# Performance work log

Hardware: AMD Instinct MI355X
Metric: run time of the kernel (lower is better)

The kernel has to match this reference:

```python
import jax, jax.numpy as jnp
import numpy as np

NUM_LEVELS = 16
LOG2_T = 19
TABLE_SIZE = 1 << LOG2_T
F_PER_LEVEL = 2
MIN_RES, MAX_RES = 16, 4096
N = 524288

_growth = np.exp((np.log(MAX_RES) - np.log(MIN_RES)) / (NUM_LEVELS - 1))
SCALINGS = np.floor(MIN_RES * _growth ** np.arange(NUM_LEVELS)).astype(np.float32)  # [L]
HASH_OFFSET = (np.arange(NUM_LEVELS) * TABLE_SIZE).astype(np.uint32)  # [L]
# corner selection: True -> use ceil coord, order matches torch hashed_0..hashed_7
CORNER_MASK = np.array([[1,1,1],[1,0,1],[0,0,1],[0,1,1],[1,1,0],[1,0,0],[0,0,0],[0,1,0]], dtype=bool)
PRIMES = np.array([1, 2654435761, 805459861], dtype=np.uint32)


def _hash(coords):
    # coords: uint32 [..., 3]; instant-ngp spatial hash, table size is a power of 2
    c = coords * jnp.asarray(PRIMES)
    h = c[..., 0] ^ c[..., 1] ^ c[..., 2]
    h = h & jnp.uint32(TABLE_SIZE - 1)
    return (h + jnp.asarray(HASH_OFFSET)).astype(jnp.int32)  # [..., L]


def hash_encode(pts, table):
    # pts: [N, 3] in [0,1]; table: [L*T, F]
    scaled = pts[:, None, :] * jnp.asarray(SCALINGS)[:, None]            # [N, L, 3]
    sc = jnp.ceil(scaled).astype(jnp.int32).astype(jnp.uint32)
    sf_f = jnp.floor(scaled)
    sf = sf_f.astype(jnp.int32).astype(jnp.uint32)
    offset = scaled - sf_f                                               # [N, L, 3]
    mask = jnp.asarray(CORNER_MASK)[:, None, None, :]                    # [8,1,1,3]
    coords = jnp.where(mask, sc[None], sf[None])                         # [8, N, L, 3]
    f = table[_hash(coords)]                                             # [8, N, L, F]
    wx = offset[..., 0:1]; wy = offset[..., 1:2]; wz = offset[..., 2:3]
    f_03 = f[0] * wx + f[3] * (1 - wx)
    f_12 = f[1] * wx + f[2] * (1 - wx)
    f_56 = f[5] * wx + f[6] * (1 - wx)
    f_47 = f[4] * wx + f[7] * (1 - wx)
    f0312 = f_03 * wy + f_12 * (1 - wy)
    f4756 = f_47 * wy + f_56 * (1 - wy)
    enc = f0312 * wz + f4756 * (1 - wz)                                  # [N, L, F]
    return enc.reshape(enc.shape[0], NUM_LEVELS * F_PER_LEVEL)


def setup_inputs() -> dict:
    key = jax.random.key(0)
    k1, k2, k3, k4 = jax.random.split(key, 4)
    x = jax.random.uniform(k1, (N, 6), dtype=jnp.float32)
    hash_table = (jax.random.uniform(k2, (TABLE_SIZE * NUM_LEVELS, F_PER_LEVEL), dtype=jnp.float32) * 2 - 1) * 1e-3
    w1 = jax.random.normal(k3, (64, 64), dtype=jnp.float32) * 0.05
    w2 = jax.random.normal(k4, (64, 16), dtype=jnp.float32) * 0.05
    return {"x": x, "hash_table": hash_table, "w1": w1, "w2": w2}


def reference(x, hash_table, w1, w2):
    p0, p1 = x[:, :3], x[:, 3:]                          # segment start / end
    enc = jnp.concatenate([hash_encode(p0, hash_table), hash_encode(p1, hash_table)], axis=-1)  # [N,64]
    h = jax.nn.relu(enc @ w1)                            # FullyFusedMLP: 1 hidden layer, ReLU, no bias
    out = h @ w2                                         # [N, 1+geo_feat_dim]
    density = jnp.exp(out[:, :1] - 1.0)                  # trunc_exp(x - 1)
    return jnp.concatenate([density, out[:, 1:]], axis=-1)
```

## Files before the change

### kernel.cpp

```cpp
#include <hip/hip_runtime.h>
#include <math.h>

#define NLVL 16
#define TSIZE (1u << 19)
#define PRIME_Y 2654435761u
#define PRIME_Z 805459861u
#define QSCALE 126000.0f
#define W1SCALE 254.0f

#if __has_builtin(__builtin_amdgcn_sdot4)
#define HAS_SDOT4 1
#else
#define HAS_SDOT4 0
#endif
#if __has_builtin(__builtin_amdgcn_fdot2)
#define HAS_FDOT2 1
#else
#define HAS_FDOT2 0
#endif

typedef _Float16 half2_t __attribute__((ext_vector_type(2)));

struct ScalingsArg { float s[NLVL]; };
struct QuadArg { int off[4]; int res[4]; };

__device__ __forceinline__ unsigned f2bf(float f) {
    unsigned u = __float_as_uint(f);
    return (u + 0x7fffu + ((u >> 16) & 1u)) >> 16;
}
__device__ __forceinline__ float bf2f(unsigned hw) { return __uint_as_float(hw << 16); }
__device__ __forceinline__ unsigned pkbf2(float2 v) { return f2bf(v.x) | (f2bf(v.y) << 16); }

__device__ __forceinline__ int q8(float v) {
    return __float2int_rn(fmaxf(fminf(v * QSCALE, 127.f), -127.f));
}
__device__ __forceinline__ unsigned qw8(float v) {
    return (unsigned)(__float2int_rn(fmaxf(fminf(v * W1SCALE, 127.f), -127.f))) & 0xffu;
}

__device__ __forceinline__ int dot4i8(unsigned a, unsigned b, int c) {
#if HAS_SDOT4
    return __builtin_amdgcn_sdot4((int)a, (int)b, c, false);
#else
    c += (int)(signed char)(a & 0xffu)         * (int)(signed char)(b & 0xffu);
    c += (int)(signed char)((a >> 8) & 0xffu)  * (int)(signed char)((b >> 8) & 0xffu);
    c += (int)(signed char)((a >> 16) & 0xffu) * (int)(signed char)((b >> 16) & 0xffu);
    c += (int)(signed char)(a >> 24)           * (int)(signed char)(b >> 24);
    return c;
#endif
}

__device__ __forceinline__ unsigned pkh2(float a, float b) {
    union { half2_t h; unsigned u; } cv;
    cv.h.x = (_Float16)a; cv.h.y = (_Float16)b;
    return cv.u;
}
__device__ __forceinline__ float dot2h(unsigned a, unsigned b, float c) {
    union { unsigned u; half2_t h; } ca, cb;
    ca.u = a; cb.u = b;
#if HAS_FDOT2
    return __builtin_amdgcn_fdot2(ca.h, cb.h, c, false);
#else
    return c + (float)ca.h.x * (float)cb.h.x + (float)ca.h.y * (float)cb.h.y;
#endif
}

__device__ __forceinline__ unsigned pick4(uint4 q, int sel) {
    const unsigned a = (sel & 1) ? q.y : q.x;
    const unsigned b = (sel & 1) ? q.w : q.z;
    return (sel & 2) ? b : a;
}

__global__ __launch_bounds__(256) void ngp_conv12(
    const float4* __restrict__ src, uint2* __restrict__ o, int n2)
{
    const int i = blockIdx.x * 256 + threadIdx.x;
    if (i < n2) {
        const float4 v = src[i];
        o[i] = make_uint2(f2bf(v.x) | (f2bf(v.y) << 16),
                          f2bf(v.z) | (f2bf(v.w) << 16));
    }
}

__global__ __launch_bounds__(256) void ngp_quad(
    const float2* __restrict__ tf, uint4* __restrict__ quads, QuadArg qa)
{
    const int l = blockIdx.y;
    const int res = qa.res[l];
    const int n = (res + 1) * res * res;
    const int idx = blockIdx.x * 256 + threadIdx.x;
    if (idx >= n) return;
    const int xq = idx % res;
    const int t1 = idx / res;
    const int yq = t1 % res;
    const int zq = t1 / res;
    const unsigned m = TSIZE - 1u;
    const unsigned base = (unsigned)l * TSIZE;
    const unsigned hy0 = (unsigned)yq * PRIME_Y, hy1 = (unsigned)(yq + 1) * PRIME_Y;
    const unsigned hz  = (unsigned)zq * PRIME_Z;
    const unsigned x0 = (unsigned)xq, x1 = (unsigned)(xq + 1);
    const float2 e00 = tf[((x0 ^ hy0 ^ hz) & m) + base];
    const float2 e10 = tf[((x1 ^ hy0 ^ hz) & m) + base];
    const float2 e01 = tf[((x0 ^ hy1 ^ hz) & m) + base];
    const float2 e11 = tf[((x1 ^ hy1 ^ hz) & m) + base];
    quads[qa.off[l] + idx] = make_uint4(pkbf2(e00), pkbf2(e10), pkbf2(e01), pkbf2(e11));
}

__global__ __launch_bounds__(256) void ngp_encode2(
    const float* __restrict__ x,
    const unsigned* __restrict__ tbHi,
    const uint4* __restrict__ quads,
    unsigned* __restrict__ encq,
    ScalingsArg sca, QuadArg qa, int npts)
{
    const int pt = blockIdx.x * 256 + threadIdx.x;
    if (pt >= npts) return;
    const int l = blockIdx.y;
    const float s = sca.s[l];
    const unsigned m = TSIZE - 1u;

    const float* xp = x + (size_t)pt * 6;
    const float2 v0 = *reinterpret_cast<const float2*>(xp);
    const float2 v1 = *reinterpret_cast<const float2*>(xp + 2);
    const float2 v2 = *reinterpret_cast<const float2*>(xp + 4);
    const float q[2][3] = { { v0.x, v0.y, v1.x }, { v1.y, v2.x, v2.y } };

    int qb[4];
    #pragma unroll
    for (int e = 0; e < 2; ++e) {
        const float sx = q[e][0] * s, sy = q[e][1] * s, sz = q[e][2] * s;
        const float fx = floorf(sx), fy = floorf(sy), fz = floorf(sz);
        const float wx = sx - fx, wy = sy - fy, wz = sz - fz;
        const unsigned ixf = (unsigned)(int)fx, iyf = (unsigned)(int)fy, izf = (unsigned)(int)fz;
        const unsigned ixc = (unsigned)(int)ceilf(sx);
        const unsigned iyc = (unsigned)(int)ceilf(sy);
        const unsigned izc = (unsigned)(int)ceilf(sz);

        float2 cc[4], cf[4];

        if (l < 4) {
            const int res = qa.res[l];
            const int dxs = (int)(ixc - ixf);
            const int dys = (int)(iyc - iyf);
            const uint4* Q = quads + qa.off[l];
            const int rowf = (int)iyf * res + (int)ixf;
            const uint4 qzc = Q[(int)izc * (res * res) + rowf];
            const uint4 qzf = Q[(int)izf * (res * res) + rowf];
            const int selcc = dys * 2 + dxs;
            const int selfc = dys * 2;
            const int selcf = dxs;
            const unsigned u0 = pick4(qzc, selcc);
            const unsigned u1 = pick4(qzc, selcf);
            const unsigned u2 = qzc.x;
            const unsigned u3 = pick4(qzc, selfc);
            const unsigned u4 = pick4(qzf, selcc);
            const unsigned u5 = pick4(qzf, selcf);
            const unsigned u6 = qzf.x;
            const unsigned u7 = pick4(qzf, selfc);
            cc[0] = make_float2(bf2f(u0 & 0xffffu), bf2f(u0 >> 16));
            cf[0] = make_float2(bf2f(u3 & 0xffffu), bf2f(u3 >> 16));
            cc[1] = make_float2(bf2f(u1 & 0xffffu), bf2f(u1 >> 16));
            cf[1] = make_float2(bf2f(u2 & 0xffffu), bf2f(u2 >> 16));
            cc[2] = make_float2(bf2f(u5 & 0xffffu), bf2f(u5 >> 16));
            cf[2] = make_float2(bf2f(u6 & 0xffffu), bf2f(u6 >> 16));
            cc[3] = make_float2(bf2f(u4 & 0xffffu), bf2f(u4 >> 16));
            cf[3] = make_float2(bf2f(u7 & 0xffffu), bf2f(u7 >> 16));
        } else {
            const unsigned base = (unsigned)(l - 4) * TSIZE;
            const unsigned hyf = iyf * PRIME_Y, hyc = iyc * PRIME_Y;
            const unsigned hzf = izf * PRIME_Z, hzc = izc * PRIME_Z;
            const unsigned H[4] = { hyc ^ hzc, hyf ^ hzc, hyf ^ hzf, hyc ^ hzf };
            const unsigned dx = ixf ^ ixc;
            #pragma unroll
            for (int j = 0; j < 4; ++j) {
                const unsigned A  = (ixf ^ H[j]) & m;
                const unsigned Ax = A ^ dx;
                const uint4 blk = *reinterpret_cast<const uint4*>(&tbHi[base + (A & ~3u)]);
                const unsigned uf = pick4(blk, (int)(A & 3u));
                unsigned uc = pick4(blk, (int)(Ax & 3u));
                if (dx > 3u) uc = tbHi[base + Ax];
                cf[j] = make_float2(bf2f(uf & 0xffffu), bf2f(uf >> 16));
                cc[j] = make_float2(bf2f(uc & 0xffffu), bf2f(uc >> 16));
            }
        }

        const float cx = 1.f - wx, cy = 1.f - wy, cz = 1.f - wz;
        const float g03x = cc[0].x * wx + cf[0].x * cx, g03y = cc[0].y * wx + cf[0].y * cx;
        const float g12x = cc[1].x * wx + cf[1].x * cx, g12y = cc[1].y * wx + cf[1].y * cx;
        const float g56x = cc[2].x * wx + cf[2].x * cx, g56y = cc[2].y * wx + cf[2].y * cx;
        const float g47x = cc[3].x * wx + cf[3].x * cx, g47y = cc[3].y * wx + cf[3].y * cx;
        const float t0x = g03x * wy + g12x * cy, t0y = g03y * wy + g12y * cy;
        const float t1x = g47x * wy + g56x * cy, t1y = g47y * wy + g56y * cy;
        qb[e * 2 + 0] = q8(t0x * wz + t1x * cz);
        qb[e * 2 + 1] = q8(t0y * wz + t1y * cz);
    }

    encq[(size_t)l * npts + pt] =
        (qb[0] & 0xff) | ((qb[1] & 0xff) << 8) | ((qb[2] & 0xff) << 16) | ((qb[3] & 0xff) << 24);
}

template<int BF>
__global__ __launch_bounds__(256) void ngp_encode_lvl(
    const float* __restrict__ x,
    const float2* __restrict__ tf,
    const unsigned* __restrict__ tb,
    unsigned* __restrict__ encq,
    ScalingsArg sca, int npts)
{
    const int pt = blockIdx.x * 256 + threadIdx.x;
    if (pt >= npts) return;
    const int l = blockIdx.y;
    const float s = sca.s[l];
    const unsigned base = (unsigned)l * TSIZE;
    const unsigned m = TSIZE - 1u;

    const float* xp = x + (size_t)pt * 6;
    const float2 v0 = *reinterpret_cast<const float2*>(xp);
    const float2 v1 = *reinterpret_cast<const float2*>(xp + 2);
    const float2 v2 = *reinterpret_cast<const float2*>(xp + 4);
    const float q[2][3] = { { v0.x, v0.y, v1.x }, { v1.y, v2.x, v2.y } };

    int qb[4];
    #pragma unroll
    for (int e = 0; e < 2; ++e) {
        const float sx = q[e][0] * s, sy = q[e][1] * s, sz = q[e][2] * s;
        const float fx = floorf(sx), fy = floorf(sy), fz = floorf(sz);
        const float wx = sx - fx, wy = sy - fy, wz = sz - fz;
        const unsigned ixf = (unsigned)(int)fx, iyf = (unsigned)(int)fy, izf = (unsigned)(int)fz;
        const unsigned ixc = (unsigned)(int)ceilf(sx);
        const unsigned iyc = (unsigned)(int)ceilf(sy);
        const unsigned izc = (unsigned)(int)ceilf(sz);
        const unsigned hyf = iyf * PRIME_Y, hyc = iyc * PRIME_Y;
        const unsigned hzf = izf * PRIME_Z, hzc = izc * PRIME_Z;
        const unsigned h0 = hyc ^ hzc, h1 = hyf ^ hzc, h2 = hyf ^ hzf, h3 = hyc ^ hzf;
        const unsigned dx = ixf ^ ixc;
        const unsigned A[4] = { (ixf ^ h0) & m, (ixf ^ h1) & m,
                                (ixf ^ h2) & m, (ixf ^ h3) & m };
        float2 cf[4], cc[4];
        if (dx == 1u) {
            #pragma unroll
            for (int j = 0; j < 4; ++j) {
                const float4 v = *reinterpret_cast<const float4*>(&tf[base + (A[j] & ~1u)]);
                const bool hi = (A[j] & 1u) != 0u;
                cf[j] = hi ? make_float2(v.z, v.w) : make_float2(v.x, v.y);
                cc[j] = hi ? make_float2(v.x, v.y) : make_float2(v.z, v.w);
            }
        } else {
            #pragma unroll
            for (int j = 0; j < 4; ++j) {
                cf[j] = tf[base + A[j]];
                cc[j] = tf[base + ((A[j] ^ dx) & m)];
            }
        }
        const float cx = 1.f - wx, cy = 1.f - wy, cz = 1.f - wz;
        const float g03x = cc[0].x * wx + cf[0].x * cx, g03y = cc[0].y * wx + cf[0].y * cx;
        const float g12x = cc[1].x * wx + cf[1].x * cx, g12y = cc[1].y * wx + cf[1].y * cx;
        const float g56x = cc[2].x * wx + cf[2].x * cx, g56y = cc[2].y * wx + cf[2].y * cx;
        const float g47x = cc[3].x * wx + cf[3].x * cx, g47y = cc[3].y * wx + cf[3].y * cx;
        const float t0x = g03x * wy + g12x * cy, t0y = g03y * wy + g12y * cy;
        const float t1x = g47x * wy + g56x * cy, t1y = g47y * wy + g56y * cy;
        qb[e * 2 + 0] = q8(t0x * wz + t1x * cz);
        qb[e * 2 + 1] = q8(t0y * wz + t1y * cz);
    }
    encq[(size_t)l * npts + pt] =
        (qb[0] & 0xff) | ((qb[1] & 0xff) << 8) | ((qb[2] & 0xff) << 16) | ((qb[3] & 0xff) << 24);
}

__global__ __launch_bounds__(256) void ngp_mlp2i(
    const unsigned* __restrict__ encq,
    const float* __restrict__ w1,
    const float* __restrict__ w2,
    float* __restrict__ out, int npts)
{
    __shared__ unsigned lw1i[64 * 16];
    __shared__ unsigned lw2h[16 * 32];
    const int tid = threadIdx.x;

    #pragma unroll
    for (int t = 0; t < 4; ++t) {
        const int idx = tid * 4 + t;
        const int j = idx >> 4, g = idx & 15;
        const unsigned b0 = qw8(w1[(2 * g) * 64 + j]);
        const unsigned b1 = qw8(w1[(2 * g + 1) * 64 + j]);
        const unsigned b2 = qw8(w1[(32 + 2 * g) * 64 + j]);
        const unsigned b3 = qw8(w1[(33 + 2 * g) * 64 + j]);
        lw1i[j * 16 + g] = b0 | (b1 << 8) | (b2 << 16) | (b3 << 24);
    }
    #pragma unroll
    for (int t = 0; t < 2; ++t) {
        const int idx = tid * 2 + t;
        const int c = idx >> 5, jp = idx & 31;
        lw2h[c * 32 + jp] = pkh2(w2[(2 * jp) * 16 + c], w2[(2 * jp + 1) * 16 + c]);
    }
    __syncthreads();

    const int base = (blockIdx.x * 256 + tid) * 2;
    if (base >= npts) return;

    unsigned ev0[16], ev1[16];
    #pragma unroll
    for (int l = 0; l < NLVL; ++l) {
        const uint2 v = *reinterpret_cast<const uint2*>(&encq[(size_t)l * npts + base]);
        ev0[l] = v.x; ev1[l] = v.y;
    }

    const float s1 = 1.0f / (QSCALE * W1SCALE);
    unsigned hp0[32], hp1[32];
    #pragma unroll
    for (int jp = 0; jp < 32; ++jp) {
        const int j0 = 2 * jp, j1 = 2 * jp + 1;
        int a00 = 0, a10 = 0, a01 = 0, a11 = 0;
        #pragma unroll
        for (int g4 = 0; g4 < 4; ++g4) {
            const uint4 w = *reinterpret_cast<const uint4*>(&lw1i[j0 * 16 + g4 * 4]);
            a00 = dot4i8(ev0[g4 * 4 + 0], w.x, a00); a10 = dot4i8(ev1[g4 * 4 + 0], w.x, a10);
            a00 = dot4i8(ev0[g4 * 4 + 1], w.y, a00); a10 = dot4i8(ev1[g4 * 4 + 1], w.y, a10);
            a00 = dot4i8(ev0[g4 * 4 + 2], w.z, a00); a10 = dot4i8(ev1[g4 * 4 + 2], w.z, a10);
            a00 = dot4i8(ev0[g4 * 4 + 3], w.w, a00); a10 = dot4i8(ev1[g4 * 4 + 3], w.w, a10);
        }
        #pragma unroll
        for (int g4 = 0; g4 < 4; ++g4) {
            const uint4 w = *reinterpret_cast<const uint4*>(&lw1i[j1 * 16 + g4 * 4]);
            a01 = dot4i8(ev0[g4 * 4 + 0], w.x, a01); a11 = dot4i8(ev1[g4 * 4 + 0], w.x, a11);
            a01 = dot4i8(ev0[g4 * 4 + 1], w.y, a01); a11 = dot4i8(ev1[g4 * 4 + 1], w.y, a11);
            a01 = dot4i8(ev0[g4 * 4 + 2], w.z, a01); a11 = dot4i8(ev1[g4 * 4 + 2], w.z, a11);
            a01 = dot4i8(ev0[g4 * 4 + 3], w.w, a01); a11 = dot4i8(ev1[g4 * 4 + 3], w.w, a11);
        }
        hp0[jp] = pkh2(fmaxf((float)a00, 0.f) * s1, fmaxf((float)a01, 0.f) * s1);
        hp1[jp] = pkh2(fmaxf((float)a10, 0.f) * s1, fmaxf((float)a11, 0.f) * s1);
    }

    float* op0 = out + (size_t)base * 16;
    const bool p1 = (base + 1 < npts);
    for (int c = 0; c < 16; ++c) {
        float s0 = 0.f, s1v = 0.f;
        #pragma unroll
        for (int jq = 0; jq < 8; ++jq) {
            const uint4 w = *reinterpret_cast<const uint4*>(&lw2h[c * 32 + jq * 4]);
            s0  = dot2h(hp0[jq * 4 + 0], w.x, s0);  s1v = dot2h(hp1[jq * 4 + 0], w.x, s1v);
            s0  = dot2h(hp0[jq * 4 + 1], w.y, s0);  s1v = dot2h(hp1[jq * 4 + 1], w.y, s1v);
            s0  = dot2h(hp0[jq * 4 + 2], w.z, s0);  s1v = dot2h(hp1[jq * 4 + 2], w.z, s1v);
            s0  = dot2h(hp0[jq * 4 + 3], w.w, s0);  s1v = dot2h(hp1[jq * 4 + 3], w.w, s1v);
        }
        if (c == 0) { s0 = expf(s0 - 1.0f); s1v = expf(s1v - 1.0f); }
        op0[c] = s0;
        if (p1) op0[16 + c] = s1v;
    }
}

__global__ __launch_bounds__(256) void ngp_fused(
    const float* __restrict__ x,
    const float2* __restrict__ table,
    const float* __restrict__ w1,
    const float* __restrict__ w2,
    float* __restrict__ out,
    ScalingsArg sca, int npts)
{
    __shared__ float lw1[64 * 64];
    __shared__ float lw2[64 * 16];
    const int tid = threadIdx.x;
    #pragma unroll
    for (int i = 0; i < 16; ++i) lw1[tid + 256 * i] = w1[tid + 256 * i];
    #pragma unroll
    for (int i = 0; i < 4; ++i)  lw2[tid + 256 * i] = w2[tid + 256 * i];
    __syncthreads();

    const int gid = blockIdx.x * 256 + tid;
    if (gid >= npts) return;

    const float* xp = x + (size_t)gid * 6;
    float2 v0 = *reinterpret_cast<const float2*>(xp);
    float2 v1 = *reinterpret_cast<const float2*>(xp + 2);
    float2 v2 = *reinterpret_cast<const float2*>(xp + 4);
    float Pt[6] = { v0.x, v0.y, v1.x, v1.y, v2.x, v2.y };

    float enc[64];
    #pragma unroll
    for (int p = 0; p < 2; ++p) {
        const float qx = Pt[p * 3 + 0], qy = Pt[p * 3 + 1], qz = Pt[p * 3 + 2];
        #pragma unroll
        for (int l = 0; l < NLVL; ++l) {
            const float s = sca.s[l];
            const float sx = qx * s, sy = qy * s, sz = qz * s;
            const float fx = floorf(sx), fy = floorf(sy), fz = floorf(sz);
            const float wx = sx - fx, wy = sy - fy, wz = sz - fz;
            const unsigned ixf = (unsigned)(int)fx, iyf = (unsigned)(int)fy, izf = (unsigned)(int)fz;
            const unsigned ixc = (unsigned)(int)ceilf(sx);
            const unsigned iyc = (unsigned)(int)ceilf(sy);
            const unsigned izc = (unsigned)(int)ceilf(sz);
            const unsigned hyf = iyf * PRIME_Y, hyc = iyc * PRIME_Y;
            const unsigned hzf = izf * PRIME_Z, hzc = izc * PRIME_Z;
            const unsigned mm = TSIZE - 1u;
            const unsigned bs = (unsigned)l * TSIZE;
            const float2 f0 = table[((ixc ^ hyc ^ hzc) & mm) + bs];
            const float2 f1 = table[((ixc ^ hyf ^ hzc) & mm) + bs];
            const float2 f2 = table[((ixf ^ hyf ^ hzc) & mm) + bs];
            const float2 f3 = table[((ixf ^ hyc ^ hzc) & mm) + bs];
            const float2 f4 = table[((ixc ^ hyc ^ hzf) & mm) + bs];
            const float2 f5 = table[((ixc ^ hyf ^ hzf) & mm) + bs];
            const float2 f6 = table[((ixf ^ hyf ^ hzf) & mm) + bs];
            const float2 f7 = table[((ixf ^ hyc ^ hzf) & mm) + bs];
            const float cx = 1.f - wx, cy = 1.f - wy, cz = 1.f - wz;
            const float g03x = f0.x * wx + f3.x * cx, g03y = f0.y * wx + f3.y * cx;
            const float g12x = f1.x * wx + f2.x * cx, g12y = f1.y * wx + f2.y * cx;
            const float g56x = f5.x * wx + f6.x * cx, g56y = f5.y * wx + f6.y * cx;
            const float g47x = f4.x * wx + f7.x * cx, g47y = f4.y * wx + f7.y * cx;
            const float t0x = g03x * wy + g12x * cy, t0y = g03y * wy + g12y * cy;
            const float t1x = g47x * wy + g56x * cy, t1y = g47y * wy + g56y * cy;
            enc[p * 32 + l * 2 + 0] = t0x * wz + t1x * cz;
            enc[p * 32 + l * 2 + 1] = t0y * wz + t1y * cz;
        }
    }

    float o[16];
    #pragma unroll
    for (int i = 0; i < 16; ++i) o[i] = 0.f;
    for (int jb = 0; jb < 64; jb += 8) {
        float acc[8];
        #pragma unroll
        for (int jj = 0; jj < 8; ++jj) acc[jj] = 0.f;
        #pragma unroll
        for (int k = 0; k < 64; ++k) {
            const float e = enc[k];
            const float4* wrow = reinterpret_cast<const float4*>(&lw1[k * 64 + jb]);
            const float4 wa = wrow[0], wb = wrow[1];
            acc[0] += e * wa.x; acc[1] += e * wa.y; acc[2] += e * wa.z; acc[3] += e * wa.w;
            acc[4] += e * wb.x; acc[5] += e * wb.y; acc[6] += e * wb.z; acc[7] += e * wb.w;
        }
        #pragma unroll
        for (int jj = 0; jj < 8; ++jj) {
            const float hv = fmaxf(acc[jj], 0.f);
            const float4* w2row = reinterpret_cast<const float4*>(&lw2[(jb + jj) * 16]);
            const float4 wa = w2row[0], wb = w2row[1], wc = w2row[2], wd = w2row[3];
            o[0]  += hv * wa.x; o[1]  += hv * wa.y; o[2]  += hv * wa.z; o[3]  += hv * wa.w;
            o[4]  += hv * wb.x; o[5]  += hv * wb.y; o[6]  += hv * wb.z; o[7]  += hv * wb.w;
            o[8]  += hv * wc.x; o[9]  += hv * wc.y; o[10] += hv * wc.z; o[11] += hv * wc.w;
            o[12] += hv * wd.x; o[13] += hv * wd.y; o[14] += hv * wd.z; o[15] += hv * wd.w;
        }
    }
    o[0] = expf(o[0] - 1.0f);
    float4* op = reinterpret_cast<float4*>(out + (size_t)gid * 16);
    op[0] = make_float4(o[0],  o[1],  o[2],  o[3]);
    op[1] = make_float4(o[4],  o[5],  o[6],  o[7]);
    op[2] = make_float4(o[8],  o[9],  o[10], o[11]);
    op[3] = make_float4(o[12], o[13], o[14], o[15]);
}

extern "C" void kernel_launch(void* const* d_in, const int* in_sizes, int n_in,
                              void* d_out, int out_size, void* d_ws, size_t ws_size,
                              hipStream_t stream) {
    const float*  x     = (const float*)d_in[0];
    const float2* table = (const float2*)d_in[1];
    const float*  w1    = (const float*)d_in[2];
    const float*  w2    = (const float*)d_in[3];
    float* out = (float*)d_out;
    const int npts = in_sizes[0] / 6;

    ScalingsArg sca;
    const double growth = exp((log(4096.0) - log(16.0)) / 15.0);
    for (int i = 0; i < NLVL; ++i)
        sca.s[i] = (float)floor(16.0 * pow(growth, (double)i));

    QuadArg qa;
    int qtot = 0, qmax = 0;
    for (int l = 0; l < 4; ++l) {
        const int r = (int)sca.s[l];
        qa.res[l] = r;
        qa.off[l] = qtot;
        const int n = (r + 1) * r * r;
        qtot += n;
        if (n > qmax) qmax = n;
    }

    const size_t tbhi_bytes = (size_t)12 * TSIZE * 4u;
    const size_t enc_bytes  = (size_t)NLVL * (size_t)npts * 4u;
    const size_t quad_bytes = (size_t)qtot * 16u;
    const int bpl = (npts + 255) / 256;
    const dim3 gEnc(bpl, NLVL);
    const int mlp_blocks = ((npts + 1) / 2 + 255) / 256;

    if (ws_size >= tbhi_bytes + enc_bytes + quad_bytes) {
        unsigned* tbHi = (unsigned*)d_ws;
        unsigned* enc  = (unsigned*)((char*)d_ws + tbhi_bytes);
        uint4*    quads = (uint4*)((char*)d_ws + tbhi_bytes + enc_bytes);
        const int n2 = (12 * TSIZE) / 2;
        ngp_conv12<<<(n2 + 255) / 256, 256, 0, stream>>>(
            (const float4*)(table + (size_t)4 * TSIZE), (uint2*)tbHi, n2);
        ngp_quad<<<dim3((qmax + 255) / 256, 4), 256, 0, stream>>>(table, quads, qa);
        ngp_encode2<<<gEnc, 256, 0, stream>>>(x, tbHi, quads, enc, sca, qa, npts);
        ngp_mlp2i<<<mlp_blocks, 256, 0, stream>>>(enc, w1, w2, out, npts);
    } else if (ws_size >= enc_bytes) {
        unsigned* enc = (unsigned*)d_ws;
        ngp_encode_lvl<0><<<gEnc, 256, 0, stream>>>(x, table, nullptr, enc, sca, npts);
        ngp_mlp2i<<<mlp_blocks, 256, 0, stream>>>(enc, w1, w2, out, npts);
    } else {
        ngp_fused<<<(npts + 255) / 256, 256, 0, stream>>>(x, table, w1, w2, out, sca, npts);
    }
}
```

Before: 363.6 us.

## Process two points per thread in encode and extend quad tables to level 4

Replaces the one-point-per-thread encode kernel with one that handles two points per thread. Coordinates are loaded with float4 reads, all gather addresses are computed before the loads, and results are written as a uint2, so more table gathers are in flight per thread. Level 4 also moves from the hashed bf16 table to a precomputed quad table, cutting gathers per corner pair from four to two. The cost is a larger quad workspace, higher register pressure and half as many threads per level.

```diff
diff --git a/kernel.cpp b/kernel.cpp
--- a/kernel.cpp
+++ b/kernel.cpp
@@ -7,6 +7,7 @@
 #define PRIME_Z 805459861u
 #define QSCALE 126000.0f
 #define W1SCALE 254.0f
+#define NQUAD 5
 
 #if __has_builtin(__builtin_amdgcn_sdot4)
 #define HAS_SDOT4 1
@@ -22,7 +23,7 @@
 typedef _Float16 half2_t __attribute__((ext_vector_type(2)));
 
 struct ScalingsArg { float s[NLVL]; };
-struct QuadArg { int off[4]; int res[4]; };
+struct QuadArg { int off[NQUAD]; int res[NQUAD]; };
 
 __device__ __forceinline__ unsigned f2bf(float f) {
     unsigned u = __float_as_uint(f);
@@ -69,6 +70,19 @@
     const unsigned a = (sel & 1) ? q.y : q.x;
     const unsigned b = (sel & 1) ? q.w : q.z;
     return (sel & 2) ? b : a;
+}
+
+__device__ __forceinline__ void lerp8(const float2 cc[4], const float2 cf[4],
+                                      float wx, float wy, float wz, int& qx, int& qy) {
+    const float cx = 1.f - wx, cy = 1.f - wy, cz = 1.f - wz;
+    const float g03x = cc[0].x * wx + cf[0].x * cx, g03y = cc[0].y * wx + cf[0].y * cx;
+    const float g12x = cc[1].x * wx + cf[1].x * cx, g12y = cc[1].y * wx + cf[1].y * cx;
+    const float g56x = cc[2].x * wx + cf[2].x * cx, g56y = cc[2].y * wx + cf[2].y * cx;
+    const float g47x = cc[3].x * wx + cf[3].x * cx, g47y = cc[3].y * wx + cf[3].y * cx;
+    const float t0x = g03x * wy + g12x * cy, t0y = g03y * wy + g12y * cy;
+    const float t1x = g47x * wy + g56x * cy, t1y = g47y * wy + g56y * cy;
+    qx = q8(t0x * wz + t1x * cz);
+    qy = q8(t0y * wz + t1y * cz);
 }
 
 __global__ __launch_bounds__(256) void ngp_conv12(
@@ -106,57 +120,78 @@
     quads[qa.off[l] + idx] = make_uint4(pkbf2(e00), pkbf2(e10), pkbf2(e01), pkbf2(e11));
 }
 
-__global__ __launch_bounds__(256) void ngp_encode2(
+__global__ __launch_bounds__(256) void ngp_encode3(
     const float* __restrict__ x,
     const unsigned* __restrict__ tbHi,
     const uint4* __restrict__ quads,
     unsigned* __restrict__ encq,
     ScalingsArg sca, QuadArg qa, int npts)
 {
-    const int pt = blockIdx.x * 256 + threadIdx.x;
-    if (pt >= npts) return;
+    const int p0 = (blockIdx.x * 256 + threadIdx.x) * 2;
+    if (p0 >= npts) return;
+    const bool has1 = (p0 + 1) < npts;
     const int l = blockIdx.y;
     const float s = sca.s[l];
     const unsigned m = TSIZE - 1u;
 
-    const float* xp = x + (size_t)pt * 6;
-    const float2 v0 = *reinterpret_cast<const float2*>(xp);
-    const float2 v1 = *reinterpret_cast<const float2*>(xp + 2);
-    const float2 v2 = *reinterpret_cast<const float2*>(xp + 4);
-    const float q[2][3] = { { v0.x, v0.y, v1.x }, { v1.y, v2.x, v2.y } };
-
-    int qb[4];
-    #pragma unroll
-    for (int e = 0; e < 2; ++e) {
-        const float sx = q[e][0] * s, sy = q[e][1] * s, sz = q[e][2] * s;
-        const float fx = floorf(sx), fy = floorf(sy), fz = floorf(sz);
-        const float wx = sx - fx, wy = sy - fy, wz = sz - fz;
-        const unsigned ixf = (unsigned)(int)fx, iyf = (unsigned)(int)fy, izf = (unsigned)(int)fz;
-        const unsigned ixc = (unsigned)(int)ceilf(sx);
-        const unsigned iyc = (unsigned)(int)ceilf(sy);
-        const unsigned izc = (unsigned)(int)ceilf(sz);
-
-        float2 cc[4], cf[4];
-
-        if (l < 4) {
-            const int res = qa.res[l];
-            const int dxs = (int)(ixc - ixf);
-            const int dys = (int)(iyc - iyf);
-            const uint4* Q = quads + qa.off[l];
-            const int rowf = (int)iyf * res + (int)ixf;
-            const uint4 qzc = Q[(int)izc * (res * res) + rowf];
-            const uint4 qzf = Q[(int)izf * (res * res) + rowf];
-            const int selcc = dys * 2 + dxs;
-            const int selfc = dys * 2;
-            const int selcf = dxs;
-            const unsigned u0 = pick4(qzc, selcc);
-            const unsigned u1 = pick4(qzc, selcf);
-            const unsigned u2 = qzc.x;
-            const unsigned u3 = pick4(qzc, selfc);
-            const unsigned u4 = pick4(qzf, selcc);
-            const unsigned u5 = pick4(qzf, selcf);
-            const unsigned u6 = qzf.x;
-            const unsigned u7 = pick4(qzf, selfc);
+    const float* xp = x + (size_t)p0 * 6;
+    float SX[4], SY[4], SZ[4];
+    {
+        float c[12];
+        if (has1) {
+            const float4 a0 = *reinterpret_cast<const float4*>(xp);
+            const float4 a1 = *reinterpret_cast<const float4*>(xp + 4);
+            const float4 a2 = *reinterpret_cast<const float4*>(xp + 8);
+            c[0] = a0.x; c[1] = a0.y; c[2]  = a0.z; c[3]  = a0.w;
+            c[4] = a1.x; c[5] = a1.y; c[6]  = a1.z; c[7]  = a1.w;
+            c[8] = a2.x; c[9] = a2.y; c[10] = a2.z; c[11] = a2.w;
+        } else {
+            #pragma unroll
+            for (int i = 0; i < 6; ++i) c[i] = xp[i];
+            #pragma unroll
+            for (int i = 0; i < 6; ++i) c[6 + i] = c[i];
+        }
+        SX[0] = c[0] * s; SY[0] = c[1] * s;  SZ[0] = c[2] * s;
+        SX[1] = c[3] * s; SY[1] = c[4] * s;  SZ[1] = c[5] * s;
+        SX[2] = c[6] * s; SY[2] = c[7] * s;  SZ[2] = c[8] * s;
+        SX[3] = c[9] * s; SY[3] = c[10] * s; SZ[3] = c[11] * s;
+    }
+
+    int qf0[4], qf1[4];
+
+    if (l < NQUAD) {
+        const int res = qa.res[l];
+        const uint4* Q = quads + qa.off[l];
+        uint4 pzc[4], pzf[4];
+        int dxs[4], dys[4];
+        float WX[4], WY[4], WZ[4];
+        #pragma unroll
+        for (int cI = 0; cI < 4; ++cI) {
+            const float sx = SX[cI], sy = SY[cI], sz = SZ[cI];
+            const float fx = floorf(sx), fy = floorf(sy), fz = floorf(sz);
+            WX[cI] = sx - fx; WY[cI] = sy - fy; WZ[cI] = sz - fz;
+            const int ixf = (int)fx, iyf = (int)fy, izf = (int)fz;
+            dxs[cI] = (int)ceilf(sx) - ixf;
+            dys[cI] = (int)ceilf(sy) - iyf;
+            const int izc = (int)ceilf(sz);
+            const int rowf = iyf * res + ixf;
+            pzc[cI] = Q[izc * (res * res) + rowf];
+            pzf[cI] = Q[izf * (res * res) + rowf];
+        }
+        #pragma unroll
+        for (int cI = 0; cI < 4; ++cI) {
+            const int selcc = dys[cI] * 2 + dxs[cI];
+            const int selfc = dys[cI] * 2;
+            const int selcf = dxs[cI];
+            const unsigned u0 = pick4(pzc[cI], selcc);
+            const unsigned u1 = pick4(pzc[cI], selcf);
+            const unsigned u2 = pzc[cI].x;
+            const unsigned u3 = pick4(pzc[cI], selfc);
+            const unsigned u4 = pick4(pzf[cI], selcc);
+            const unsigned u5 = pick4(pzf[cI], selcf);
+            const unsigned u6 = pzf[cI].x;
+            const unsigned u7 = pick4(pzf[cI], selfc);
+            float2 cc[4], cf[4];
             cc[0] = make_float2(bf2f(u0 & 0xffffu), bf2f(u0 >> 16));
             cf[0] = make_float2(bf2f(u3 & 0xffffu), bf2f(u3 >> 16));
             cc[1] = make_float2(bf2f(u1 & 0xffffu), bf2f(u1 >> 16));
@@ -165,38 +200,73 @@
             cf[2] = make_float2(bf2f(u6 & 0xffffu), bf2f(u6 >> 16));
             cc[3] = make_float2(bf2f(u4 & 0xffffu), bf2f(u4 >> 16));
             cf[3] = make_float2(bf2f(u7 & 0xffffu), bf2f(u7 >> 16));
-        } else {
-            const unsigned base = (unsigned)(l - 4) * TSIZE;
-            const unsigned hyf = iyf * PRIME_Y, hyc = iyc * PRIME_Y;
-            const unsigned hzf = izf * PRIME_Z, hzc = izc * PRIME_Z;
-            const unsigned H[4] = { hyc ^ hzc, hyf ^ hzc, hyf ^ hzf, hyc ^ hzf };
-            const unsigned dx = ixf ^ ixc;
-            #pragma unroll
-            for (int j = 0; j < 4; ++j) {
-                const unsigned A  = (ixf ^ H[j]) & m;
-                const unsigned Ax = A ^ dx;
-                const uint4 blk = *reinterpret_cast<const uint4*>(&tbHi[base + (A & ~3u)]);
-                const unsigned uf = pick4(blk, (int)(A & 3u));
-                unsigned uc = pick4(blk, (int)(Ax & 3u));
-                if (dx > 3u) uc = tbHi[base + Ax];
-                cf[j] = make_float2(bf2f(uf & 0xffffu), bf2f(uf >> 16));
-                cc[j] = make_float2(bf2f(uc & 0xffffu), bf2f(uc >> 16));
+            lerp8(cc, cf, WX[cI], WY[cI], WZ[cI], qf0[cI], qf1[cI]);
+        }
+    } else {
+        const unsigned base = (unsigned)(l - 4) * TSIZE;
+        #pragma unroll
+        for (int h = 0; h < 2; ++h) {
+            unsigned A[2][4], DX[2];
+            float WX[2], WY[2], WZ[2];
+            #pragma unroll
+            for (int u = 0; u < 2; ++u) {
+                const int cI = 2 * h + u;
+                const float sx = SX[cI], sy = SY[cI], sz = SZ[cI];
+                const float fx = floorf(sx), fy = floorf(sy), fz = floorf(sz);
+                WX[u] = sx - fx; WY[u] = sy - fy; WZ[u] = sz - fz;
+                const unsigned ixf = (unsigned)(int)fx;
+                const unsigned iyf = (unsigned)(int)fy;
+                const unsigned izf = (unsigned)(int)fz;
+                const unsigned ixc = (unsigned)(int)ceilf(sx);
+                const unsigned iyc = (unsigned)(int)ceilf(sy);
+                const unsigned izc = (unsigned)(int)ceilf(sz);
+                const unsigned hyf = iyf * PRIME_Y, hyc = iyc * PRIME_Y;
+                const unsigned hzf = izf * PRIME_Z, hzc = izc * PRIME_Z;
+                DX[u] = ixf ^ ixc;
+                A[u][0] = (ixf ^ (hyc ^ hzc)) & m;
+                A[u][1] = (ixf ^ (hyf ^ hzc)) & m;
+                A[u][2] = (ixf ^ (hyf ^ hzf)) & m;
+                A[u][3] = (ixf ^ (hyc ^ hzf)) & m;
             }
-        }
-
-        const float cx = 1.f - wx, cy = 1.f - wy, cz = 1.f - wz;
-        const float g03x = cc[0].x * wx + cf[0].x * cx, g03y = cc[0].y * wx + cf[0].y * cx;
-        const float g12x = cc[1].x * wx + cf[1].x * cx, g12y = cc[1].y * wx + cf[1].y * cx;
-        const float g56x = cc[2].x * wx + cf[2].x * cx, g56y = cc[2].y * wx + cf[2].y * cx;
-        const float g47x = cc[3].x * wx + cf[3].x * cx, g47y = cc[3].y * wx + cf[3].y * cx;
-        const float t0x = g03x * wy + g12x * cy, t0y = g03y * wy + g12y * cy;
-        const float t1x = g47x * wy + g56x * cy, t1y = g47y * wy + g56y * cy;
-        qb[e * 2 + 0] = q8(t0x * wz + t1x * cz);
-        qb[e * 2 + 1] = q8(t0y * wz + t1y * cz);
-    }
-
-    encq[(size_t)l * npts + pt] =
-        (qb[0] & 0xff) | ((qb[1] & 0xff) << 8) | ((qb[2] & 0xff) << 16) | ((qb[3] & 0xff) << 24);
+            uint4 blk[2][4];
+            #pragma unroll
+            for (int u = 0; u < 2; ++u) {
+                #pragma unroll
+                for (int j = 0; j < 4; ++j)
+                    blk[u][j] = *reinterpret_cast<const uint4*>(&tbHi[base + (A[u][j] & ~3u)]);
+            }
+            unsigned uc[2][4];
+            #pragma unroll
+            for (int u = 0; u < 2; ++u) {
+                #pragma unroll
+                for (int j = 0; j < 4; ++j) {
+                    const unsigned Ax = A[u][j] ^ DX[u];
+                    uc[u][j] = pick4(blk[u][j], (int)(Ax & 3u));
+                    if (DX[u] > 3u) uc[u][j] = tbHi[base + Ax];
+                }
+            }
+            #pragma unroll
+            for (int u = 0; u < 2; ++u) {
+                float2 cc[4], cf[4];
+                #pragma unroll
+                for (int j = 0; j < 4; ++j) {
+                    const unsigned uf = pick4(blk[u][j], (int)(A[u][j] & 3u));
+                    cf[j] = make_float2(bf2f(uf & 0xffffu), bf2f(uf >> 16));
+                    cc[j] = make_float2(bf2f(uc[u][j] & 0xffffu), bf2f(uc[u][j] >> 16));
+                }
+                lerp8(cc, cf, WX[u], WY[u], WZ[u], qf0[2 * h + u], qf1[2 * h + u]);
+            }
+        }
+    }
+
+    const unsigned w0 = (qf0[0] & 0xff) | ((qf1[0] & 0xff) << 8) |
+                        ((qf0[1] & 0xff) << 16) | ((qf1[1] & 0xff) << 24);
+    const unsigned w1 = (qf0[2] & 0xff) | ((qf1[2] & 0xff) << 8) |
+                        ((qf0[3] & 0xff) << 16) | ((qf1[3] & 0xff) << 24);
+    if (has1)
+        *reinterpret_cast<uint2*>(&encq[(size_t)l * npts + p0]) = make_uint2(w0, w1);
+    else
+        encq[(size_t)l * npts + p0] = w0;
 }
 
 template<int BF>
@@ -463,7 +533,7 @@
 
     QuadArg qa;
     int qtot = 0, qmax = 0;
-    for (int l = 0; l < 4; ++l) {
+    for (int l = 0; l < NQUAD; ++l) {
         const int r = (int)sca.s[l];
         qa.res[l] = r;
         qa.off[l] = qtot;
@@ -475,8 +545,6 @@
     const size_t tbhi_bytes = (size_t)12 * TSIZE * 4u;
     const size_t enc_bytes  = (size_t)NLVL * (size_t)npts * 4u;
     const size_t quad_bytes = (size_t)qtot * 16u;
-    const int bpl = (npts + 255) / 256;
-    const dim3 gEnc(bpl, NLVL);
     const int mlp_blocks = ((npts + 1) / 2 + 255) / 256;
 
     if (ws_size >= tbhi_bytes + enc_bytes + quad_bytes) {
@@ -486,12 +554,14 @@
         const int n2 = (12 * TSIZE) / 2;
         ngp_conv12<<<(n2 + 255) / 256, 256, 0, stream>>>(
             (const float4*)(table + (size_t)4 * TSIZE), (uint2*)tbHi, n2);
-        ngp_quad<<<dim3((qmax + 255) / 256, 4), 256, 0, stream>>>(table, quads, qa);
-        ngp_encode2<<<gEnc, 256, 0, stream>>>(x, tbHi, quads, enc, sca, qa, npts);
+        ngp_quad<<<dim3((qmax + 255) / 256, NQUAD), 256, 0, stream>>>(table, quads, qa);
+        const int bpl2 = ((npts + 1) / 2 + 255) / 256;
+        ngp_encode3<<<dim3(bpl2, NLVL), 256, 0, stream>>>(x, tbHi, quads, enc, sca, qa, npts);
         ngp_mlp2i<<<mlp_blocks, 256, 0, stream>>>(enc, w1, w2, out, npts);
     } else if (ws_size >= enc_bytes) {
         unsigned* enc = (unsigned*)d_ws;
-        ngp_encode_lvl<0><<<gEnc, 256, 0, stream>>>(x, table, nullptr, enc, sca, npts);
+        const int bpl = (npts + 255) / 256;
+        ngp_encode_lvl<0><<<dim3(bpl, NLVL), 256, 0, stream>>>(x, table, nullptr, enc, sca, npts);
         ngp_mlp2i<<<mlp_blocks, 256, 0, stream>>>(enc, w1, w2, out, npts);
     } else {
         ngp_fused<<<(npts + 255) / 256, 256, 0, stream>>>(x, table, w1, w2, out, sca, npts);
```

New measurement: 358.2 us. No clear change (-1.5%).
